# Performance work log

Hardware: AMD Instinct MI355X
Metric: run time of the kernel (lower is better)

Reference implementation:

```python
import jax, jax.numpy as jnp
import numpy as np

H = 128      # num_hidden
HIN = 384    # num_in (h_E feature dim)
DFF = 512    # FFN inner dim = 4*H
SCALE = 30.0
EPS = 1e-5

def gelu(x):
    return jax.nn.gelu(x, approximate=False)

def linear(x, w, b):
    return x @ w.T + b

def layer_norm(x, w, b):
    mu = jnp.mean(x, axis=-1, keepdims=True)
    var = jnp.var(x, axis=-1, keepdims=True)
    return (x - mu) * jax.lax.rsqrt(var + EPS) * w + b


def setup_inputs() -> dict:
    key = jax.random.key(0)
    ks = jax.random.split(key, 10)
    B, N, K = 4, 2048, 48
    s = lambda d: 1.0 / np.sqrt(d)
    return {
        "h_V": jax.random.normal(ks[0], (B, N, H), jnp.float32),
        "h_E": jax.random.normal(ks[1], (B, N, K, HIN), jnp.float32),
        "mask_V": jnp.ones((B, N), jnp.float32),
        "mask_attend": jnp.ones((B, N, K), jnp.float32),
        "W1_w": jax.random.normal(ks[2], (H, H + HIN), jnp.float32) * s(H + HIN),
        "W1_b": jnp.zeros((H,), jnp.float32),
        "W2_w": jax.random.normal(ks[3], (H, H), jnp.float32) * s(H),
        "W2_b": jnp.zeros((H,), jnp.float32),
        "W3_w": jax.random.normal(ks[4], (H, H), jnp.float32) * s(H),
        "W3_b": jnp.zeros((H,), jnp.float32),
        "ln1_w": jnp.ones((H,), jnp.float32),
        "ln1_b": jnp.zeros((H,), jnp.float32),
        "Win_w": jax.random.normal(ks[5], (DFF, H), jnp.float32) * s(H),
        "Win_b": jnp.zeros((DFF,), jnp.float32),
        "Wout_w": jax.random.normal(ks[6], (H, DFF), jnp.float32) * s(DFF),
        "Wout_b": jnp.zeros((H,), jnp.float32),
        "ln2_w": jnp.ones((H,), jnp.float32),
        "ln2_b": jnp.zeros((H,), jnp.float32),
    }


def reference(h_V, h_E, mask_V, mask_attend,
              W1_w, W1_b, W2_w, W2_b, W3_w, W3_b,
              ln1_w, ln1_b, Win_w, Win_b, Wout_w, Wout_b, ln2_w, ln2_b):
    K = h_E.shape[-2]
    # broadcast node feats to neighbors and concat: [B, N, K, H+HIN]
    h_V_expand = jnp.broadcast_to(h_V[:, :, None, :], (*h_V.shape[:2], K, h_V.shape[-1]))
    h_EV = jnp.concatenate([h_V_expand, h_E], axis=-1)
    h_message = linear(gelu(linear(gelu(linear(h_EV, W1_w, W1_b)), W2_w, W2_b)), W3_w, W3_b)
    h_message = mask_attend[..., None] * h_message
    dh = jnp.sum(h_message, axis=-2) / SCALE
    h = layer_norm(h_V + dh, ln1_w, ln1_b)
    dh = linear(gelu(linear(h, Win_w, Win_b)), Wout_w, Wout_b)
    h = layer_norm(h + dh, ln2_w, ln2_b)
    return mask_V[..., None] * h
```

## Files before the change

kernel.cpp:

```cpp
#include <hip/hip_runtime.h>
#include <hip/hip_bf16.h>

#define H    128
#define HIN  384
#define FIN  512
#define KNB  48
#define DFF  512
#define NNODES 8192
#define NNB_F (KNB*HIN)

typedef float f32x4 __attribute__((ext_vector_type(4)));
typedef short bf16x8 __attribute__((ext_vector_type(8)));

__device__ __forceinline__ short bfs(float x){
  __hip_bfloat16 h = __float2bfloat16(x);
  return *(short*)&h;
}

__device__ __forceinline__ bf16x8 pack8(float4 a, float4 b){
  bf16x8 o;
  o[0]=bfs(a.x); o[1]=bfs(a.y); o[2]=bfs(a.z); o[3]=bfs(a.w);
  o[4]=bfs(b.x); o[5]=bfs(b.y); o[6]=bfs(b.z); o[7]=bfs(b.w);
  return o;
}

__device__ __forceinline__ float gelu_f(float x){
  return 0.5f * x * (1.0f + erff(x * 0.70710678118654752f));
}

__device__ __forceinline__ f32x4 zero4(){ f32x4 z; z[0]=0.f;z[1]=0.f;z[2]=0.f;z[3]=0.f; return z; }

__global__ __launch_bounds__(256) void k_convert(
    const float* __restrict__ W1, const float* __restrict__ W2,
    const float* __restrict__ W3, const float* __restrict__ Win,
    const float* __restrict__ Wout, unsigned short* __restrict__ dst)
{
  int i0 = (blockIdx.x*256 + threadIdx.x)*4;
  #pragma unroll
  for (int t=0;t<4;t++){
    int idx = i0 + t;
    float v;
    if      (idx <  65536) v = W1[idx];
    else if (idx <  81920) v = W2[idx-65536];
    else if (idx <  98304) v = W3[idx-81920];
    else if (idx < 163840) v = Win[idx-98304];
    else                   v = Wout[idx-163840];
    dst[idx] = (unsigned short)bfs(v);
  }
}

__global__ __launch_bounds__(256) void k_bias1(
    const float* __restrict__ hV, const unsigned short* __restrict__ wW1,
    const float* __restrict__ W1b, float* __restrict__ bias1)
{
  int tid = threadIdx.x;
  int wid = tid>>6, lane = tid&63;
  int lr = lane&15, lg = lane>>4;
  int m0 = (blockIdx.x*4 + wid)*16;

  f32x4 acc[8];
  #pragma unroll
  for (int i=0;i<8;i++) acc[i] = zero4();

  #pragma unroll
  for (int ks=0; ks<4; ks++){
    const float* p = hV + (size_t)(m0+lr)*H + ks*32 + lg*8;
    bf16x8 a = pack8(*(const float4*)p, *(const float4*)(p+4));
    #pragma unroll
    for (int nt=0; nt<8; nt++){
      bf16x8 b = *(const bf16x8*)(wW1 + (size_t)(nt*16+lr)*FIN + ks*32 + lg*8);
      acc[nt] = __builtin_amdgcn_mfma_f32_16x16x32_bf16(a, b, acc[nt], 0,0,0);
    }
  }
  #pragma unroll
  for (int nt=0; nt<8; nt++){
    int col = nt*16 + lr;
    float bv = W1b[col];
    #pragma unroll
    for (int e=0;e<4;e++){
      int row = lg*4 + e;
      bias1[(size_t)(m0+row)*H + col] = acc[nt][e] + bv;
    }
  }
}

__global__ __launch_bounds__(256) void k_message(
    const float* __restrict__ hV, const float* __restrict__ hE,
    const float* __restrict__ maskA,
    const unsigned short* __restrict__ wW1, const unsigned short* __restrict__ wW2,
    const unsigned short* __restrict__ wW3,
    const float* __restrict__ W2b, const float* __restrict__ W3b,
    const float* __restrict__ ln1w, const float* __restrict__ ln1b,
    const float* __restrict__ bias1, float* __restrict__ hmid)
{
  __shared__ __align__(16) unsigned short sA[2][48*136];
  __shared__ __align__(16) unsigned short sG[48*136];
  __shared__ float sMask[48];
  __shared__ float sBias[128];
  __shared__ float sDh[128];

  int node = blockIdx.x;
  int tid  = threadIdx.x;
  const float* hEn = hE + (size_t)node * NNB_F;

  int wid = tid>>6, lane = tid&63;
  int lr = lane&15, lg = lane>>4;

  int sr = tid>>4, scg = tid&15;
  const float* gp = hEn + (size_t)sr*HIN + scg*8;

  float4 c0[3][2], c1[3][2], c2[3][2];
  #pragma unroll
  for (int i=0;i<3;i++){
    const float* p = gp + i*16*HIN;
    c0[i][0] = *(const float4*)(p);       c0[i][1] = *(const float4*)(p+4);
  }
  #pragma unroll
  for (int i=0;i<3;i++){
    const float* p = gp + i*16*HIN + 128;
    c1[i][0] = *(const float4*)(p);       c1[i][1] = *(const float4*)(p+4);
  }
  #pragma unroll
  for (int i=0;i<3;i++){
    const float* p = gp + i*16*HIN + 256;
    c2[i][0] = *(const float4*)(p);       c2[i][1] = *(const float4*)(p+4);
  }
  if (tid < 48)  sMask[tid] = maskA[(size_t)node*KNB + tid];
  if (tid < 128) sBias[tid] = bias1[(size_t)node*H + tid];
  #pragma unroll
  for (int i=0;i<3;i++)
    *(bf16x8*)(&sA[0][(sr+16*i)*136 + scg*8]) = pack8(c0[i][0], c0[i][1]);
  __syncthreads();

  f32x4 acc1[3][2];
  #pragma unroll
  for (int mt=0;mt<3;mt++){ acc1[mt][0]=zero4(); acc1[mt][1]=zero4(); }

  auto gemm1_chunk = [&](const unsigned short* buf, int c){
    #pragma unroll
    for (int ks=0; ks<4; ks++){
      bf16x8 a[3];
      #pragma unroll
      for (int mt=0;mt<3;mt++)
        a[mt] = *(const bf16x8*)(buf + (mt*16+lr)*136 + ks*32 + lg*8);
      #pragma unroll
      for (int j=0;j<2;j++){
        int nt = wid*2 + j;
        bf16x8 b = *(const bf16x8*)(wW1 + (size_t)(nt*16+lr)*FIN + (H + c*128 + ks*32 + lg*8));
        #pragma unroll
        for (int mt=0;mt<3;mt++)
          acc1[mt][j] = __builtin_amdgcn_mfma_f32_16x16x32_bf16(a[mt], b, acc1[mt][j], 0,0,0);
      }
    }
  };

  gemm1_chunk(sA[0], 0);
  #pragma unroll
  for (int i=0;i<3;i++)
    *(bf16x8*)(&sA[1][(sr+16*i)*136 + scg*8]) = pack8(c1[i][0], c1[i][1]);
  __syncthreads();

  gemm1_chunk(sA[1], 1);
  #pragma unroll
  for (int i=0;i<3;i++)
    *(bf16x8*)(&sA[0][(sr+16*i)*136 + scg*8]) = pack8(c2[i][0], c2[i][1]);
  __syncthreads();

  gemm1_chunk(sA[0], 2);
  __syncthreads();

  #pragma unroll
  for (int j=0;j<2;j++){
    int col = (wid*2+j)*16 + lr;
    float bv = sBias[col];
    #pragma unroll
    for (int mt=0;mt<3;mt++){
      #pragma unroll
      for (int e=0;e<4;e++){
        float g = gelu_f(acc1[mt][j][e] + bv);
        int row = mt*16 + lg*4 + e;
        sG[row*136 + col] = (unsigned short)bfs(g);
      }
    }
  }
  __syncthreads();

  f32x4 acc2[3][2];
  #pragma unroll
  for (int mt=0;mt<3;mt++){ acc2[mt][0]=zero4(); acc2[mt][1]=zero4(); }
  #pragma unroll
  for (int ks=0; ks<4; ks++){
    bf16x8 a[3];
    #pragma unroll
    for (int mt=0;mt<3;mt++)
      a[mt] = *(const bf16x8*)(sG + (mt*16+lr)*136 + ks*32 + lg*8);
    #pragma unroll
    for (int j=0;j<2;j++){
      int nt = wid*2 + j;
      bf16x8 b = *(const bf16x8*)(wW2 + (size_t)(nt*16+lr)*H + ks*32 + lg*8);
      #pragma unroll
      for (int mt=0;mt<3;mt++)
        acc2[mt][j] = __builtin_amdgcn_mfma_f32_16x16x32_bf16(a[mt], b, acc2[mt][j], 0,0,0);
    }
  }
  __syncthreads();

  #pragma unroll
  for (int j=0;j<2;j++){
    int col = (wid*2+j)*16 + lr;
    float bv = W2b[col];
    #pragma unroll
    for (int mt=0;mt<3;mt++){
      #pragma unroll
      for (int e=0;e<4;e++){
        float g = gelu_f(acc2[mt][j][e] + bv);
        int row = mt*16 + lg*4 + e;
        sG[row*136 + col] = (unsigned short)bfs(g);
      }
    }
  }
  __syncthreads();

  f32x4 acc3[3][2];
  #pragma unroll
  for (int mt=0;mt<3;mt++){ acc3[mt][0]=zero4(); acc3[mt][1]=zero4(); }
  #pragma unroll
  for (int ks=0; ks<4; ks++){
    bf16x8 a[3];
    #pragma unroll
    for (int mt=0;mt<3;mt++)
      a[mt] = *(const bf16x8*)(sG + (mt*16+lr)*136 + ks*32 + lg*8);
    #pragma unroll
    for (int j=0;j<2;j++){
      int nt = wid*2 + j;
      bf16x8 b = *(const bf16x8*)(wW3 + (size_t)(nt*16+lr)*H + ks*32 + lg*8);
      #pragma unroll
      for (int mt=0;mt<3;mt++)
        acc3[mt][j] = __builtin_amdgcn_mfma_f32_16x16x32_bf16(a[mt], b, acc3[mt][j], 0,0,0);
    }
  }
  #pragma unroll
  for (int j=0;j<2;j++){
    int col = (wid*2+j)*16 + lr;
    float bv = W3b[col];
    float p = 0.f;
    #pragma unroll
    for (int mt=0;mt<3;mt++){
      #pragma unroll
      for (int e=0;e<4;e++){
        int row = mt*16 + lg*4 + e;
        p += (acc3[mt][j][e] + bv) * sMask[row];
      }
    }
    p += __shfl_xor(p, 16);
    p += __shfl_xor(p, 32);
    if (lane < 16) sDh[(wid*2+j)*16 + lane] = p;
  }
  __syncthreads();

  if (wid == 0){
    int c0i = lane, c1i = lane + 64;
    float t0 = hV[(size_t)node*H + c0i] + sDh[c0i]*(1.0f/30.0f);
    float t1 = hV[(size_t)node*H + c1i] + sDh[c1i]*(1.0f/30.0f);
    float s = t0 + t1, q = t0*t0 + t1*t1;
    #pragma unroll
    for (int off=1; off<64; off<<=1){ s += __shfl_xor(s, off); q += __shfl_xor(q, off); }
    float mu  = s * (1.0f/128.0f);
    float var = q * (1.0f/128.0f) - mu*mu;
    float rs  = rsqrtf(var + 1e-5f);
    hmid[(size_t)node*H + c0i] = (t0-mu)*rs*ln1w[c0i] + ln1b[c0i];
    hmid[(size_t)node*H + c1i] = (t1-mu)*rs*ln1w[c1i] + ln1b[c1i];
  }
}

__global__ __launch_bounds__(256) void k_ffn(
    const float* __restrict__ hmid, const unsigned short* __restrict__ wWin,
    const unsigned short* __restrict__ wWout,
    const float* __restrict__ Winb, const float* __restrict__ Woutb,
    const float* __restrict__ ln2w, const float* __restrict__ ln2b,
    const float* __restrict__ maskV, float* __restrict__ out)
{
  __shared__ __align__(16) unsigned short sH[32*136];
  __shared__ __align__(16) unsigned short sU[32*520];
  __shared__ float sT[32*132];

  int tid = threadIdx.x;
  int m0 = blockIdx.x * 32;

  #pragma unroll
  for (int i=0;i<2;i++){
    int c = i*256 + tid;
    int row = c>>4, cir = c&15;
    const float* p = hmid + (size_t)(m0+row)*H + cir*8;
    *(bf16x8*)(sH + row*136 + cir*8) = pack8(*(const float4*)p, *(const float4*)(p+4));
  }
  __syncthreads();

  int wid = tid>>6, lane = tid&63;
  int lr = lane&15, lg = lane>>4;

  f32x4 acc[2][8];
  #pragma unroll
  for (int mt=0;mt<2;mt++)
    #pragma unroll
    for (int j=0;j<8;j++) acc[mt][j] = zero4();

  #pragma unroll
  for (int ks=0; ks<4; ks++){
    bf16x8 a[2];
    #pragma unroll
    for (int mt=0;mt<2;mt++)
      a[mt] = *(const bf16x8*)(sH + (mt*16+lr)*136 + ks*32 + lg*8);
    #pragma unroll
    for (int j=0;j<8;j++){
      int nt = wid*8 + j;
      bf16x8 b = *(const bf16x8*)(wWin + (size_t)(nt*16+lr)*H + ks*32 + lg*8);
      #pragma unroll
      for (int mt=0;mt<2;mt++)
        acc[mt][j] = __builtin_amdgcn_mfma_f32_16x16x32_bf16(a[mt], b, acc[mt][j], 0,0,0);
    }
  }
  #pragma unroll
  for (int j=0;j<8;j++){
    int col = (wid*8+j)*16 + lr;
    float bv = Winb[col];
    #pragma unroll
    for (int mt=0;mt<2;mt++){
      #pragma unroll
      for (int e=0;e<4;e++){
        float g = gelu_f(acc[mt][j][e] + bv);
        int row = mt*16 + lg*4 + e;
        sU[row*520 + col] = (unsigned short)bfs(g);
      }
    }
  }
  __syncthreads();

  f32x4 accO[2][2];
  #pragma unroll
  for (int mt=0;mt<2;mt++){ accO[mt][0]=zero4(); accO[mt][1]=zero4(); }

  for (int ks=0; ks<16; ks++){
    bf16x8 a[2];
    #pragma unroll
    for (int mt=0;mt<2;mt++)
      a[mt] = *(const bf16x8*)(sU + (mt*16+lr)*520 + ks*32 + lg*8);
    #pragma unroll
    for (int j=0;j<2;j++){
      int nt = wid*2 + j;
      bf16x8 b = *(const bf16x8*)(wWout + (size_t)(nt*16+lr)*DFF + ks*32 + lg*8);
      #pragma unroll
      for (int mt=0;mt<2;mt++)
        accO[mt][j] = __builtin_amdgcn_mfma_f32_16x16x32_bf16(a[mt], b, accO[mt][j], 0,0,0);
    }
  }
  #pragma unroll
  for (int j=0;j<2;j++){
    int col = (wid*2+j)*16 + lr;
    float bv = Woutb[col];
    #pragma unroll
    for (int mt=0;mt<2;mt++){
      #pragma unroll
      for (int e=0;e<4;e++){
        int row = mt*16 + lg*4 + e;
        float t = accO[mt][j][e] + bv + hmid[(size_t)(m0+row)*H + col];
        sT[row*132 + col] = t;
      }
    }
  }
  __syncthreads();

  int row = tid>>3, part = tid&7;
  float s=0.f, q=0.f;
  #pragma unroll
  for (int jj=0;jj<16;jj++){
    float v = sT[row*132 + part*16 + jj];
    s += v; q += v*v;
  }
  s += __shfl_xor(s,1); q += __shfl_xor(q,1);
  s += __shfl_xor(s,2); q += __shfl_xor(q,2);
  s += __shfl_xor(s,4); q += __shfl_xor(q,4);
  float mu  = s*(1.0f/128.0f);
  float var = q*(1.0f/128.0f) - mu*mu;
  float rs  = rsqrtf(var + 1e-5f);
  float mv  = maskV[m0+row];
  #pragma unroll
  for (int jj=0;jj<16;jj++){
    int c = part*16 + jj;
    out[(size_t)(m0+row)*H + c] = mv * ((sT[row*132+c]-mu)*rs*ln2w[c] + ln2b[c]);
  }
}

extern "C" void kernel_launch(void* const* d_in, const int* in_sizes, int n_in,
                              void* d_out, int out_size, void* d_ws, size_t ws_size,
                              hipStream_t stream)
{
  const float* hV    = (const float*)d_in[0];
  const float* hE    = (const float*)d_in[1];
  const float* maskV = (const float*)d_in[2];
  const float* maskA = (const float*)d_in[3];
  const float* W1w   = (const float*)d_in[4];
  const float* W1b   = (const float*)d_in[5];
  const float* W2w   = (const float*)d_in[6];
  const float* W2b   = (const float*)d_in[7];
  const float* W3w   = (const float*)d_in[8];
  const float* W3b   = (const float*)d_in[9];
  const float* ln1w  = (const float*)d_in[10];
  const float* ln1b  = (const float*)d_in[11];
  const float* Winw  = (const float*)d_in[12];
  const float* Winb  = (const float*)d_in[13];
  const float* Woutw = (const float*)d_in[14];
  const float* Woutb = (const float*)d_in[15];
  const float* ln2w  = (const float*)d_in[16];
  const float* ln2b  = (const float*)d_in[17];

  unsigned short* wAll  = (unsigned short*)d_ws;
  unsigned short* wW1   = wAll;
  unsigned short* wW2   = wAll + 65536;
  unsigned short* wW3   = wAll + 81920;
  unsigned short* wWin  = wAll + 98304;
  unsigned short* wWout = wAll + 163840;
  float* bias1 = (float*)((char*)d_ws + 458752);
  float* hmid  = (float*)d_out;
  float* outp  = (float*)d_out;

  k_convert<<<224, 256, 0, stream>>>(W1w, W2w, W3w, Winw, Woutw, wAll);
  k_bias1  <<<128, 256, 0, stream>>>(hV, wW1, W1b, bias1);
  k_message<<<NNODES, 256, 0, stream>>>(hV, hE, maskA, wW1, wW2, wW3,
                                        W2b, W3b, ln1w, ln1b, bias1, hmid);
  k_ffn    <<<NNODES/32, 256, 0, stream>>>(hmid, wWin, wWout, Winb, Woutb,
                                           ln2w, ln2b, maskV, outp);
}
```

Before: 284.9 us.

## Use tanh-form GELU, stream hE chunks, reuse two LDS buffers

Replaces the erf-based GELU with a tanh-approximation expressed through exp and a fast reciprocal, cutting transcendental cost in the message MLP. The three hE chunks are now loaded into one register set just before each GEMM1 chunk instead of all up front, lowering register pressure, and launch bounds request 5 blocks per SU. LDS is cut from three buffers to two by ping-ponging GELU outputs between them, which also drops two barriers. The GELU approximation adds small numerical deviation from the exact erf form, and the later hE loads expose more memory latency per block.

```diff
diff --git a/kernel.cpp b/kernel.cpp
--- a/kernel.cpp
+++ b/kernel.cpp
@@ -25,7 +25,11 @@
 }
 
 __device__ __forceinline__ float gelu_f(float x){
-  return 0.5f * x * (1.0f + erff(x * 0.70710678118654752f));
+  float x2 = x*x;
+  float z  = x * fmaf(0.0713548162726f, x2, 1.59576912161f);
+  z = fminf(fmaxf(z, -30.f), 30.f);
+  float e = __expf(z);
+  return x * e * __builtin_amdgcn_rcpf(1.f + e);
 }
 
 __device__ __forceinline__ f32x4 zero4(){ f32x4 z; z[0]=0.f;z[1]=0.f;z[2]=0.f;z[3]=0.f; return z; }
@@ -84,7 +88,7 @@
   }
 }
 
-__global__ __launch_bounds__(256) void k_message(
+__global__ __launch_bounds__(256,5) void k_message(
     const float* __restrict__ hV, const float* __restrict__ hE,
     const float* __restrict__ maskA,
     const unsigned short* __restrict__ wW1, const unsigned short* __restrict__ wW2,
@@ -93,8 +97,8 @@
     const float* __restrict__ ln1w, const float* __restrict__ ln1b,
     const float* __restrict__ bias1, float* __restrict__ hmid)
 {
-  __shared__ __align__(16) unsigned short sA[2][48*136];
-  __shared__ __align__(16) unsigned short sG[48*136];
+  __shared__ __align__(16) unsigned short sB0[48*136];
+  __shared__ __align__(16) unsigned short sB1[48*136];
   __shared__ float sMask[48];
   __shared__ float sBias[128];
   __shared__ float sDh[128];
@@ -105,31 +109,20 @@
 
   int wid = tid>>6, lane = tid&63;
   int lr = lane&15, lg = lane>>4;
-
   int sr = tid>>4, scg = tid&15;
-  const float* gp = hEn + (size_t)sr*HIN + scg*8;
-
-  float4 c0[3][2], c1[3][2], c2[3][2];
+  const float* gp = hEn + sr*HIN + scg*8;
+
+  float4 pf[3][2];
   #pragma unroll
   for (int i=0;i<3;i++){
     const float* p = gp + i*16*HIN;
-    c0[i][0] = *(const float4*)(p);       c0[i][1] = *(const float4*)(p+4);
-  }
-  #pragma unroll
-  for (int i=0;i<3;i++){
-    const float* p = gp + i*16*HIN + 128;
-    c1[i][0] = *(const float4*)(p);       c1[i][1] = *(const float4*)(p+4);
-  }
-  #pragma unroll
-  for (int i=0;i<3;i++){
-    const float* p = gp + i*16*HIN + 256;
-    c2[i][0] = *(const float4*)(p);       c2[i][1] = *(const float4*)(p+4);
+    pf[i][0] = *(const float4*)(p); pf[i][1] = *(const float4*)(p+4);
   }
   if (tid < 48)  sMask[tid] = maskA[(size_t)node*KNB + tid];
   if (tid < 128) sBias[tid] = bias1[(size_t)node*H + tid];
   #pragma unroll
   for (int i=0;i<3;i++)
-    *(bf16x8*)(&sA[0][(sr+16*i)*136 + scg*8]) = pack8(c0[i][0], c0[i][1]);
+    *(bf16x8*)(&sB0[(sr+16*i)*136 + scg*8]) = pack8(pf[i][0], pf[i][1]);
   __syncthreads();
 
   f32x4 acc1[3][2];
@@ -154,20 +147,29 @@
     }
   };
 
-  gemm1_chunk(sA[0], 0);
+  #pragma unroll
+  for (int i=0;i<3;i++){
+    const float* p = gp + i*16*HIN + 128;
+    pf[i][0] = *(const float4*)(p); pf[i][1] = *(const float4*)(p+4);
+  }
+  gemm1_chunk(sB0, 0);
   #pragma unroll
   for (int i=0;i<3;i++)
-    *(bf16x8*)(&sA[1][(sr+16*i)*136 + scg*8]) = pack8(c1[i][0], c1[i][1]);
-  __syncthreads();
-
-  gemm1_chunk(sA[1], 1);
+    *(bf16x8*)(&sB1[(sr+16*i)*136 + scg*8]) = pack8(pf[i][0], pf[i][1]);
+  __syncthreads();
+
+  #pragma unroll
+  for (int i=0;i<3;i++){
+    const float* p = gp + i*16*HIN + 256;
+    pf[i][0] = *(const float4*)(p); pf[i][1] = *(const float4*)(p+4);
+  }
+  gemm1_chunk(sB1, 1);
   #pragma unroll
   for (int i=0;i<3;i++)
-    *(bf16x8*)(&sA[0][(sr+16*i)*136 + scg*8]) = pack8(c2[i][0], c2[i][1]);
-  __syncthreads();
-
-  gemm1_chunk(sA[0], 2);
-  __syncthreads();
+    *(bf16x8*)(&sB0[(sr+16*i)*136 + scg*8]) = pack8(pf[i][0], pf[i][1]);
+  __syncthreads();
+
+  gemm1_chunk(sB0, 2);
 
   #pragma unroll
   for (int j=0;j<2;j++){
@@ -179,7 +181,7 @@
       for (int e=0;e<4;e++){
         float g = gelu_f(acc1[mt][j][e] + bv);
         int row = mt*16 + lg*4 + e;
-        sG[row*136 + col] = (unsigned short)bfs(g);
+        sB1[row*136 + col] = (unsigned short)bfs(g);
       }
     }
   }
@@ -193,7 +195,7 @@
     bf16x8 a[3];
     #pragma unroll
     for (int mt=0;mt<3;mt++)
-      a[mt] = *(const bf16x8*)(sG + (mt*16+lr)*136 + ks*32 + lg*8);
+      a[mt] = *(const bf16x8*)(sB1 + (mt*16+lr)*136 + ks*32 + lg*8);
     #pragma unroll
     for (int j=0;j<2;j++){
       int nt = wid*2 + j;
@@ -203,8 +205,6 @@
         acc2[mt][j] = __builtin_amdgcn_mfma_f32_16x16x32_bf16(a[mt], b, acc2[mt][j], 0,0,0);
     }
   }
-  __syncthreads();
-
   #pragma unroll
   for (int j=0;j<2;j++){
     int col = (wid*2+j)*16 + lr;
@@ -215,7 +215,7 @@
       for (int e=0;e<4;e++){
         float g = gelu_f(acc2[mt][j][e] + bv);
         int row = mt*16 + lg*4 + e;
-        sG[row*136 + col] = (unsigned short)bfs(g);
+        sB0[row*136 + col] = (unsigned short)bfs(g);
       }
     }
   }
@@ -229,7 +229,7 @@
     bf16x8 a[3];
     #pragma unroll
     for (int mt=0;mt<3;mt++)
-      a[mt] = *(const bf16x8*)(sG + (mt*16+lr)*136 + ks*32 + lg*8);
+      a[mt] = *(const bf16x8*)(sB0 + (mt*16+lr)*136 + ks*32 + lg*8);
     #pragma unroll
     for (int j=0;j<2;j++){
       int nt = wid*2 + j;
```

After: 249.7 us (median of 2 runs). 1.14x faster.
